# Performance work log

Measured on AMD Instinct MI355X. Metric: run time of the kernel, lower is better.

Reference implementation:

```python
import jax, jax.numpy as jnp
import numpy as np

TEMPERATURE = 1.0

def setup_inputs() -> dict:
    key = jax.random.key(0)
    k1, k2 = jax.random.split(key)
    N, D = 8192, 128
    embeddings = jax.random.normal(k1, (N, D), dtype=jnp.float32)
    labels = jax.random.randint(k2, (N,), 0, 2, dtype=jnp.int64)
    return {"embeddings": embeddings, "labels": labels}

def reference(embeddings, labels):
    # L2-normalize rows (F.normalize p=2, dim=1)
    e = embeddings / jnp.linalg.norm(embeddings, axis=1, keepdims=True)
    N = e.shape[0]
    # scaled similarities; log of the exp'd matrix in the original is just `sim`
    sim = (e @ e.T) / TEMPERATURE            # [N, N]
    expS = jnp.exp(sim)
    eye = jnp.eye(N, dtype=bool)
    # denominator for row i: sum over all j != i of exp(sim_ij)
    # (off-diag same-class terms + all cross-class terms == all off-diag terms)
    denom = jnp.sum(jnp.where(eye, 0.0, expS), axis=1)   # [N]
    same = labels[:, None] == labels[None, :]
    pos_mask = same & ~eye                                # off-diagonal same-class pairs
    cnt = jnp.sum(pos_mask, axis=1).astype(sim.dtype)     # (#same-class - 1) per row
    # loss_i = -sum_{j in pos} (sim_ij - log denom_i)
    loss_i = -(jnp.sum(jnp.where(pos_mask, sim, 0.0), axis=1) - cnt * jnp.log(denom))
    is_pos = (labels == 0)
    num_pos = jnp.sum(is_pos).astype(sim.dtype)
    # Faithful to source: class-0 part averaged by num_pos, class-1 part added
    # un-averaged into the same accumulator; loss_neg stays 0.
    loss = jnp.sum(jnp.where(is_pos, loss_i, 0.0)) / num_pos \
         + jnp.sum(jnp.where(is_pos, 0.0, loss_i))
    return loss
```

## Files before the change

kernel.cpp:

```cpp
#include <hip/hip_runtime.h>

typedef float f32x4 __attribute__((ext_vector_type(4)));
typedef __bf16 bf16x8 __attribute__((ext_vector_type(8)));
typedef unsigned short u16x8 __attribute__((ext_vector_type(8)));

#define D_DIM 128
#define NSPLIT 32
#define SCALE  1.2011224087864498f
#define LN2    0.6931471805599453f
#define E1F    2.7182818284590452f

static __device__ __forceinline__ unsigned short f2bf(float f) {
    unsigned u = __float_as_uint(f);
    u += 0x7fffu + ((u >> 16) & 1u);
    return (unsigned short)(u >> 16);
}

__global__ __launch_bounds__(256) void prep_kernel(const float* __restrict__ X,
                                                   const int* __restrict__ labels,
                                                   unsigned short* __restrict__ A,
                                                   float* __restrict__ C,
                                                   int* __restrict__ n0) {
    int tid = threadIdx.x, wave = tid >> 6, lane = tid & 63;
    int g = lane >> 4, s = lane & 15;
    int row0 = blockIdx.x * 64;

    float c0[8], c1[8];
    #pragma unroll
    for (int e = 0; e < 8; ++e) { c0[e] = 0.f; c1[e] = 0.f; }

    #pragma unroll
    for (int it = 0; it < 4; ++it) {
        int row = row0 + wave * 16 + it * 4 + g;
        const float4* xp = reinterpret_cast<const float4*>(X + (size_t)row * D_DIM + s * 8);
        float4 xa = xp[0], xb = xp[1];
        float ss = xa.x*xa.x + xa.y*xa.y + xa.z*xa.z + xa.w*xa.w
                 + xb.x*xb.x + xb.y*xb.y + xb.z*xb.z + xb.w*xb.w;
        ss += __shfl_xor(ss, 1); ss += __shfl_xor(ss, 2);
        ss += __shfl_xor(ss, 4); ss += __shfl_xor(ss, 8);
        float rn = rsqrtf(ss) * SCALE;
        float v[8] = { xa.x*rn, xa.y*rn, xa.z*rn, xa.w*rn,
                       xb.x*rn, xb.y*rn, xb.z*rn, xb.w*rn };
        u16x8 o;
        #pragma unroll
        for (int e = 0; e < 8; ++e) o[e] = f2bf(v[e]);
        *reinterpret_cast<u16x8*>(A + (size_t)row * D_DIM + s * 8) = o;
        bool is0 = (labels[row] == 0);
        #pragma unroll
        for (int e = 0; e < 8; ++e) {
            c0[e] += is0 ? v[e] : 0.f;
            c1[e] += is0 ? 0.f : v[e];
        }
    }

    __shared__ float CL[256];
    CL[tid] = 0.f;
    __syncthreads();
    #pragma unroll
    for (int e = 0; e < 8; ++e) {
        atomicAdd(&CL[s * 8 + e],       c0[e]);
        atomicAdd(&CL[128 + s * 8 + e], c1[e]);
    }
    __syncthreads();
    atomicAdd(&C[tid], CL[tid]);

    if (wave == 0) {
        int is0 = (labels[row0 + lane] == 0) ? 1 : 0;
        unsigned long long b = __ballot(is0);
        if (lane == 0) atomicAdd(n0, (int)__popcll(b));
    }
}

__global__ __launch_bounds__(256, 3) void main_kernel(const unsigned short* __restrict__ A,
                                                      float* __restrict__ S1part,
                                                      int N) {
    int tid = threadIdx.x, wave = tid >> 6, lane = tid & 63;
    int l15 = lane & 15, lhi = lane >> 4;
    int m0 = blockIdx.x * 256 + wave * 64;
    int split = blockIdx.y;
    int jlen = N / NSPLIT;
    int j0 = split * jlen;
    int STEPS = jlen / 16;

    bf16x8 af[4][4];
    const unsigned short* abase = A + (size_t)(m0 + l15) * D_DIM + lhi * 8;
    #pragma unroll
    for (int ms = 0; ms < 4; ++ms)
        #pragma unroll
        for (int kb = 0; kb < 4; ++kb)
            af[ms][kb] = *reinterpret_cast<const bf16x8*>(abase + (size_t)ms * 16 * D_DIM + kb * 32);

    float s1[4][4];
    #pragma unroll
    for (int ms = 0; ms < 4; ++ms)
        #pragma unroll
        for (int r = 0; r < 4; ++r) s1[ms][r] = 0.f;

    const unsigned short* bbase = A + (size_t)(j0 + l15) * D_DIM + lhi * 8;
    bf16x8 bfA[4], bfB[4];
    #pragma unroll
    for (int kb = 0; kb < 4; ++kb)
        bfA[kb] = *reinterpret_cast<const bf16x8*>(bbase + kb * 32);

    for (int t = 0; t < STEPS; t += 2) {
        const unsigned short* b1 = bbase + (size_t)(t + 1) * 16 * D_DIM;
        #pragma unroll
        for (int kb = 0; kb < 4; ++kb)
            bfB[kb] = *reinterpret_cast<const bf16x8*>(b1 + kb * 32);
        {
            f32x4 acc[4] = {{0,0,0,0},{0,0,0,0},{0,0,0,0},{0,0,0,0}};
            #pragma unroll
            for (int kb = 0; kb < 4; ++kb)
                #pragma unroll
                for (int ms = 0; ms < 4; ++ms)
                    acc[ms] = __builtin_amdgcn_mfma_f32_16x16x32_bf16(af[ms][kb], bfA[kb], acc[ms], 0, 0, 0);
            #pragma unroll
            for (int ms = 0; ms < 4; ++ms)
                #pragma unroll
                for (int r = 0; r < 4; ++r)
                    s1[ms][r] += __builtin_amdgcn_exp2f(acc[ms][r]);
        }
        if (t + 2 < STEPS) {
            const unsigned short* b2 = bbase + (size_t)(t + 2) * 16 * D_DIM;
            #pragma unroll
            for (int kb = 0; kb < 4; ++kb)
                bfA[kb] = *reinterpret_cast<const bf16x8*>(b2 + kb * 32);
        }
        {
            f32x4 acc[4] = {{0,0,0,0},{0,0,0,0},{0,0,0,0},{0,0,0,0}};
            #pragma unroll
            for (int kb = 0; kb < 4; ++kb)
                #pragma unroll
                for (int ms = 0; ms < 4; ++ms)
                    acc[ms] = __builtin_amdgcn_mfma_f32_16x16x32_bf16(af[ms][kb], bfB[kb], acc[ms], 0, 0, 0);
            #pragma unroll
            for (int ms = 0; ms < 4; ++ms)
                #pragma unroll
                for (int r = 0; r < 4; ++r)
                    s1[ms][r] += __builtin_amdgcn_exp2f(acc[ms][r]);
        }
    }

    #pragma unroll
    for (int m = 1; m < 16; m <<= 1)
        #pragma unroll
        for (int ms = 0; ms < 4; ++ms)
            #pragma unroll
            for (int r = 0; r < 4; ++r)
                s1[ms][r] += __shfl_xor(s1[ms][r], m);
    if (l15 == 0) {
        #pragma unroll
        for (int ms = 0; ms < 4; ++ms)
            #pragma unroll
            for (int r = 0; r < 4; ++r)
                S1part[(size_t)split * N + m0 + ms * 16 + lhi * 4 + r] = s1[ms][r];
    }
}

__global__ __launch_bounds__(256) void finish_kernel(const float* __restrict__ S1part,
                                                     const float* __restrict__ C,
                                                     const int* __restrict__ labels,
                                                     int* __restrict__ n0p,
                                                     float* __restrict__ scal,
                                                     int* __restrict__ counter,
                                                     float* __restrict__ out,
                                                     int N) {
    int tid = threadIdx.x, wave = tid >> 6, lane = tid & 63;
    int row = blockIdx.x * 256 + tid;

    float S1 = 0.f;
    for (int s = 0; s < NSPLIT; ++s) S1 += S1part[(size_t)s * N + row];
    bool is0 = (labels[row] == 0);
    float lg = __builtin_amdgcn_logf(S1 - E1F) * LN2;
    float v0 = is0 ? lg : 0.f, v1 = is0 ? 0.f : lg;
    #pragma unroll
    for (int m = 1; m < 64; m <<= 1) { v0 += __shfl_xor(v0, m); v1 += __shfl_xor(v1, m); }

    __shared__ float red[4][2];
    __shared__ int isLast;
    if (lane == 0) { red[wave][0] = v0; red[wave][1] = v1; }
    __syncthreads();
    if (tid == 0) {
        atomicAdd(&scal[0], red[0][0] + red[1][0] + red[2][0] + red[3][0]);
        atomicAdd(&scal[1], red[0][1] + red[1][1] + red[2][1] + red[3][1]);
        __threadfence();
        int old = atomicAdd(counter, 1);
        isLast = (old == (int)gridDim.x - 1) ? 1 : 0;
    }
    __syncthreads();
    if (isLast) {
        float c = C[tid];
        float sq = c * c;
        #pragma unroll
        for (int m = 1; m < 64; m <<= 1) sq += __shfl_xor(sq, m);
        __shared__ float sqred[4];
        if (lane == 0) sqred[wave] = sq;
        __syncthreads();
        if (tid == 0) {
            float C0sq = (sqred[0] + sqred[1]) * LN2;
            float C1sq = (sqred[2] + sqred[3]) * LN2;
            float L0 = atomicAdd(&scal[0], 0.f);
            float L1 = atomicAdd(&scal[1], 0.f);
            int   n0 = atomicAdd(n0p, 0);
            float fn0 = (float)n0, fn1 = (float)(N - n0);
            float P0 = C0sq - fn0, P1 = C1sq - fn1;
            out[0] = ((fn0 - 1.f) * L0 - P0) / fn0 + (fn1 - 1.f) * L1 - P1;
        }
    }
}

extern "C" void kernel_launch(void* const* d_in, const int* in_sizes, int n_in,
                              void* d_out, int out_size, void* d_ws, size_t ws_size,
                              hipStream_t stream) {
    (void)n_in; (void)out_size; (void)ws_size;
    const float* X      = (const float*)d_in[0];
    const int*   labels = (const int*)d_in[1];
    int N = in_sizes[1];

    char* ws = (char*)d_ws;
    unsigned short* A       = (unsigned short*)ws;
    float*          S1part  = (float*)(ws + (size_t)N * D_DIM * 2);
    float*          C       = (float*)((char*)S1part + (size_t)NSPLIT * N * 4);
    float*          scal    = (float*)((char*)C + 1024);
    int*            n0      = (int*)((char*)scal + 8);
    int*            counter = n0 + 1;
    float*          out     = (float*)d_out;

    hipMemsetAsync(C, 0, 1024 + 8 + 4 + 4, stream);

    prep_kernel<<<N / 64, 256, 0, stream>>>(X, labels, A, C, n0);

    dim3 grid(N / 256, NSPLIT);
    main_kernel<<<grid, 256, 0, stream>>>(A, S1part, N);

    finish_kernel<<<N / 256, 256, 0, stream>>>(S1part, C, labels, n0, scal, counter, out, N);
}
```

Baseline: 111.3 us.

## Pack normalized embeddings in MFMA fragment order and double the column split

The prep kernel now writes the bf16 normalized embeddings in a fragment-packed layout: each 16-row tile's k-block is 512 contiguous elements, indexed by lane. The main kernel can then load each MFMA operand as one fully coalesced 16-byte-per-lane read instead of strided row reads. NSPLIT also doubles from 32 to 64, giving twice as many blocks with shorter column ranges. The cost is a larger partial-sum buffer and more work in the finish reduction.

```diff
diff --git a/kernel.cpp b/kernel.cpp
--- a/kernel.cpp
+++ b/kernel.cpp
@@ -5,7 +5,7 @@
 typedef unsigned short u16x8 __attribute__((ext_vector_type(8)));
 
 #define D_DIM 128
-#define NSPLIT 32
+#define NSPLIT 64
 #define SCALE  1.2011224087864498f
 #define LN2    0.6931471805599453f
 #define E1F    2.7182818284590452f
@@ -18,60 +18,55 @@
 
 __global__ __launch_bounds__(256) void prep_kernel(const float* __restrict__ X,
                                                    const int* __restrict__ labels,
-                                                   unsigned short* __restrict__ A,
+                                                   unsigned short* __restrict__ P,
                                                    float* __restrict__ C,
                                                    int* __restrict__ n0) {
     int tid = threadIdx.x, wave = tid >> 6, lane = tid & 63;
-    int g = lane >> 4, s = lane & 15;
-    int row0 = blockIdx.x * 64;
-
-    float c0[8], c1[8];
-    #pragma unroll
-    for (int e = 0; e < 8; ++e) { c0[e] = 0.f; c1[e] = 0.f; }
-
-    #pragma unroll
-    for (int it = 0; it < 4; ++it) {
-        int row = row0 + wave * 16 + it * 4 + g;
-        const float4* xp = reinterpret_cast<const float4*>(X + (size_t)row * D_DIM + s * 8);
-        float4 xa = xp[0], xb = xp[1];
-        float ss = xa.x*xa.x + xa.y*xa.y + xa.z*xa.z + xa.w*xa.w
-                 + xb.x*xb.x + xb.y*xb.y + xb.z*xb.z + xb.w*xb.w;
-        ss += __shfl_xor(ss, 1); ss += __shfl_xor(ss, 2);
-        ss += __shfl_xor(ss, 4); ss += __shfl_xor(ss, 8);
-        float rn = rsqrtf(ss) * SCALE;
-        float v[8] = { xa.x*rn, xa.y*rn, xa.z*rn, xa.w*rn,
-                       xb.x*rn, xb.y*rn, xb.z*rn, xb.w*rn };
+    int l15 = lane & 15, lhi = lane >> 4;
+    int jtile = blockIdx.x * 4 + wave;
+    int row = jtile * 16 + l15;
+
+    float v[4][8];
+    float ss = 0.f;
+    #pragma unroll
+    for (int kb = 0; kb < 4; ++kb) {
+        const float4* xp = reinterpret_cast<const float4*>(X + (size_t)row * D_DIM + kb * 32 + lhi * 8);
+        float4 a = xp[0], b = xp[1];
+        v[kb][0] = a.x; v[kb][1] = a.y; v[kb][2] = a.z; v[kb][3] = a.w;
+        v[kb][4] = b.x; v[kb][5] = b.y; v[kb][6] = b.z; v[kb][7] = b.w;
+        ss += a.x*a.x + a.y*a.y + a.z*a.z + a.w*a.w
+            + b.x*b.x + b.y*b.y + b.z*b.z + b.w*b.w;
+    }
+    ss += __shfl_xor(ss, 16);
+    ss += __shfl_xor(ss, 32);
+    float rn = rsqrtf(ss) * SCALE;
+    bool is0 = (labels[row] == 0);
+
+    #pragma unroll
+    for (int kb = 0; kb < 4; ++kb) {
         u16x8 o;
         #pragma unroll
-        for (int e = 0; e < 8; ++e) o[e] = f2bf(v[e]);
-        *reinterpret_cast<u16x8*>(A + (size_t)row * D_DIM + s * 8) = o;
-        bool is0 = (labels[row] == 0);
-        #pragma unroll
-        for (int e = 0; e < 8; ++e) {
-            c0[e] += is0 ? v[e] : 0.f;
-            c1[e] += is0 ? 0.f : v[e];
-        }
+        for (int e = 0; e < 8; ++e) { v[kb][e] *= rn; o[e] = f2bf(v[kb][e]); }
+        *reinterpret_cast<u16x8*>(P + ((size_t)jtile * 4 + kb) * 512 + lane * 8) = o;
     }
 
     __shared__ float CL[256];
     CL[tid] = 0.f;
     __syncthreads();
-    #pragma unroll
-    for (int e = 0; e < 8; ++e) {
-        atomicAdd(&CL[s * 8 + e],       c0[e]);
-        atomicAdd(&CL[128 + s * 8 + e], c1[e]);
-    }
+    int cbase = is0 ? 0 : 128;
+    #pragma unroll
+    for (int kb = 0; kb < 4; ++kb)
+        #pragma unroll
+        for (int e = 0; e < 8; ++e)
+            atomicAdd(&CL[cbase + kb * 32 + lhi * 8 + e], v[kb][e]);
     __syncthreads();
     atomicAdd(&C[tid], CL[tid]);
 
-    if (wave == 0) {
-        int is0 = (labels[row0 + lane] == 0) ? 1 : 0;
-        unsigned long long b = __ballot(is0);
-        if (lane == 0) atomicAdd(n0, (int)__popcll(b));
-    }
-}
-
-__global__ __launch_bounds__(256, 3) void main_kernel(const unsigned short* __restrict__ A,
+    unsigned long long b = __ballot(is0 && lhi == 0);
+    if (lane == 0) atomicAdd(n0, (int)__popcll(b));
+}
+
+__global__ __launch_bounds__(256, 3) void main_kernel(const unsigned short* __restrict__ Pk,
                                                       float* __restrict__ S1part,
                                                       int N) {
     int tid = threadIdx.x, wave = tid >> 6, lane = tid & 63;
@@ -80,15 +75,17 @@
     int split = blockIdx.y;
     int jlen = N / NSPLIT;
     int j0 = split * jlen;
-    int STEPS = jlen / 16;
+    const int STEPS = jlen / 16;
+
+    const u16x8* P = reinterpret_cast<const u16x8*>(Pk);
 
     bf16x8 af[4][4];
-    const unsigned short* abase = A + (size_t)(m0 + l15) * D_DIM + lhi * 8;
+    int fa0 = (m0 >> 4) * 4;
     #pragma unroll
     for (int ms = 0; ms < 4; ++ms)
         #pragma unroll
         for (int kb = 0; kb < 4; ++kb)
-            af[ms][kb] = *reinterpret_cast<const bf16x8*>(abase + (size_t)ms * 16 * D_DIM + kb * 32);
+            af[ms][kb] = __builtin_bit_cast(bf16x8, P[(size_t)(fa0 + ms * 4 + kb) * 64 + lane]);
 
     float s1[4][4];
     #pragma unroll
@@ -96,17 +93,16 @@
         #pragma unroll
         for (int r = 0; r < 4; ++r) s1[ms][r] = 0.f;
 
-    const unsigned short* bbase = A + (size_t)(j0 + l15) * D_DIM + lhi * 8;
+    int t0 = (j0 >> 4);
     bf16x8 bfA[4], bfB[4];
     #pragma unroll
     for (int kb = 0; kb < 4; ++kb)
-        bfA[kb] = *reinterpret_cast<const bf16x8*>(bbase + kb * 32);
+        bfA[kb] = __builtin_bit_cast(bf16x8, P[(size_t)(t0 * 4 + kb) * 64 + lane]);
 
     for (int t = 0; t < STEPS; t += 2) {
-        const unsigned short* b1 = bbase + (size_t)(t + 1) * 16 * D_DIM;
         #pragma unroll
         for (int kb = 0; kb < 4; ++kb)
-            bfB[kb] = *reinterpret_cast<const bf16x8*>(b1 + kb * 32);
+            bfB[kb] = __builtin_bit_cast(bf16x8, P[(size_t)((t0 + t + 1) * 4 + kb) * 64 + lane]);
         {
             f32x4 acc[4] = {{0,0,0,0},{0,0,0,0},{0,0,0,0},{0,0,0,0}};
             #pragma unroll
@@ -121,10 +117,9 @@
                     s1[ms][r] += __builtin_amdgcn_exp2f(acc[ms][r]);
         }
         if (t + 2 < STEPS) {
-            const unsigned short* b2 = bbase + (size_t)(t + 2) * 16 * D_DIM;
             #pragma unroll
             for (int kb = 0; kb < 4; ++kb)
-                bfA[kb] = *reinterpret_cast<const bf16x8*>(b2 + kb * 32);
+                bfA[kb] = __builtin_bit_cast(bf16x8, P[(size_t)((t0 + t + 2) * 4 + kb) * 64 + lane]);
         }
         {
             f32x4 acc[4] = {{0,0,0,0},{0,0,0,0},{0,0,0,0},{0,0,0,0}};
@@ -218,7 +213,7 @@
     int N = in_sizes[1];
 
     char* ws = (char*)d_ws;
-    unsigned short* A       = (unsigned short*)ws;
+    unsigned short* A_pack  = (unsigned short*)ws;
     float*          S1part  = (float*)(ws + (size_t)N * D_DIM * 2);
     float*          C       = (float*)((char*)S1part + (size_t)NSPLIT * N * 4);
     float*          scal    = (float*)((char*)C + 1024);
@@ -228,10 +223,10 @@
 
     hipMemsetAsync(C, 0, 1024 + 8 + 4 + 4, stream);
 
-    prep_kernel<<<N / 64, 256, 0, stream>>>(X, labels, A, C, n0);
+    prep_kernel<<<N / 64, 256, 0, stream>>>(X, labels, A_pack, C, n0);
 
     dim3 grid(N / 256, NSPLIT);
-    main_kernel<<<grid, 256, 0, stream>>>(A, S1part, N);
+    main_kernel<<<grid, 256, 0, stream>>>(A_pack, S1part, N);
 
     finish_kernel<<<N / 256, 256, 0, stream>>>(S1part, C, labels, n0, scal, counter, out, N);
 }
```

After: 104.8 us. -5.8%, faster.
